# Optimization experiments

Measured on AMD Instinct MI355X. Metric: run time of the kernel, lower is better.

The kernel has to match this reference:

```python
import jax, jax.numpy as jnp
import numpy as np

# 2x2 string of 4 cores at these (h, w) positions; ring bond topology.
POS = [(0, 0), (0, 1), (1, 0), (1, 1)]
MIN_H, MAX_H = 0, 1
MIN_W, MAX_W = 0, 1
STD = 0.9  # DumbNormalInitialization std


def setup_inputs() -> dict:
    key = jax.random.key(0)
    k1, k2 = jax.random.split(key)
    # channels: first dim = in_num_channels (2), each [B, H, W, in_quantum]
    channels = jax.random.normal(k1, (2, 8, 128, 128, 4), dtype=jnp.float32)
    # cores: [n_cores, out_quantum, bond_left, bond_right, in_q0, in_q1]
    cores = STD * jax.random.normal(k2, (4, 2, 8, 8, 4, 4), dtype=jnp.float32)
    return {"channels": channels, "cores": cores}


def reference(channels, cores):
    ch0, ch1 = channels[0], channels[1]  # each [B, H, W, Qin]
    inters = []
    for i in range(4):
        # First stage: contract core's in_quantum dims with both channels per pixel
        # -> [B, out_q, H, W, bond_l, bond_r]
        t = jnp.einsum('qlrij,bhwi,bhwj->bqhwlr', cores[i], ch0, ch1)
        h, w = POS[i]
        pad_top = MAX_H - MIN_H - (h - MIN_H)
        pad_bot = h - MIN_H
        pad_left = MAX_W - MIN_W - (w - MIN_W)
        pad_right = w - MIN_W
        # pad spatial dims with value 1.0 (multiplicative identity)
        t = jnp.pad(
            t,
            ((0, 0), (0, 0), (pad_top, pad_bot), (pad_left, pad_right), (0, 0), (0, 0)),
            constant_values=1.0,
        )
        inters.append(t)
    # Second stage: ring contraction over bond dims (i->j->k->l->i)
    out = jnp.einsum('bphwij,bqhwjk,brhwkl,bshwli->bhwpqrs', *inters)
    B, Hp, Wp = out.shape[:3]
    out = out.reshape(B, Hp, Wp, -1)  # merge out_quantum dims
    dh = MAX_H - MIN_H
    dw = MAX_W - MIN_W
    return out[:, dh:Hp - dh, dw:Wp - dw, :]
```

## Files before the change

### kernel.cpp

```cpp
#include <hip/hip_runtime.h>


typedef __fp16 h2 __attribute__((ext_vector_type(2)));
typedef __fp16 h4 __attribute__((ext_vector_type(4)));
typedef float  f4 __attribute__((ext_vector_type(4)));

#define NB 8
#define NH 128
#define NW 128
#define HO 127
#define WO 127
#define CH1_OFF (NB*NH*NW*4)
#define PXSTR 664
#define ZOFF  648
#define CDROW 68
#define CDSTR 552
#define SS    20

#define PIN() asm volatile("" ::: "memory")
#define PKRTZ(a, b) __builtin_amdgcn_cvt_pkrtz((a), (b))

__device__ __forceinline__ f4 mfma16(h4 a, h4 b, f4 c) {
  return __builtin_amdgcn_mfma_f32_16x16x16f16(a, b, c, 0, 0, 0);
}

__global__ __launch_bounds__(256, 2)
void convsbs_fused(const float* __restrict__ ch,
                   const float* __restrict__ cores,
                   float* __restrict__ out) {
  const int tid  = threadIdx.x;
  const int lane = tid & 63;
  const int wid  = tid >> 6;
  const int quad = lane >> 4;
  const int nn   = lane & 15;
  const int x8   = lane & 7;
  const f4 F4Z = {0.f, 0.f, 0.f, 0.f};

  __shared__ __align__(16) __fp16 tlds[4][8 * PXSTR];
  __shared__ __align__(16) __fp16 cdlds[4][4 * CDSTR];
  __shared__ __align__(16) float  slds[4][4 * SS];
  __fp16* tbuf = tlds[wid];
  __fp16* cdb  = cdlds[wid];
  float*  sbuf = slds[wid];

  if (lane < 8) *(h4*)(tbuf + lane * PXSTR + ZOFF) = (h4){0, 0, 0, 0};
  PIN();

  __fp16* wrbase = tbuf + nn * PXSTR + quad * 4;
  const bool wr = (nn < 8);

  h4 wf[4][8];
#pragma unroll
  for (int c = 0; c < 4; ++c)
#pragma unroll
    for (int bi = 0; bi < 8; ++bi) {
      const int rowIdx = bi * 16 + nn;
      const int q  = rowIdx >> 6;
      const int ua = (rowIdx >> 3) & 7;
      const int ub = rowIdx & 7;
      const int l = (c & 1) ? ub : ua;
      const int r = (c & 1) ? ua : ub;
      const float4 wv = *(const float4*)(
          cores + ((((c * 2 + q) * 8 + l) * 8 + r) << 4) + quad * 4);
      h2 p0 = PKRTZ(wv.x, wv.y), p1 = PKRTZ(wv.z, wv.w);
      wf[c][bi] = (h4){p0[0], p0[1], p1[0], p1[1]};
    }

  const int hq = nn >> 3, hb = nn & 7;
  const int ctA = (quad < 2) ? ((2 + hq) * 80 + hb * 8 + quad * 4) : ZOFF;
  const int ctB = (quad < 2) ? ( hq      * 80 + hb * 8 + quad * 4) : ZOFF;
  const int dA  = (quad < 2) ? ((4 + hq) * 80 + hb * 8 + quad * 4) : ZOFF;
  const int dB  = (quad < 2) ? ((6 + hq) * 80 + hb * 8 + quad * 4) : ZOFF;
  const int ctW = (hq * 2 + (quad >> 1)) * CDROW + hb * 8 + (quad & 1) * 4;
  const int dW  = (4 + (quad >> 1) * 2 + hq) * CDROW + hb * 8 + (quad & 1) * 4;
  const int eA  = (nn >> 2) * CDSTR + (nn & 3) * CDROW + quad * 4;
  const int eB  = (nn >> 2) * CDSTR + (4 + (nn & 3)) * CDROW + quad * 4;
  const bool sW = ((nn >> 2) == quad);
  const int sWo = quad * SS + (nn & 3) * 4;
  const int sRo = quad * SS + (nn & 3) * 4 + (nn >> 2);

  const int blk = blockIdx.x;
  const int b = blk / 127;
  const int y = blk - b * 127;
  const int xq = wid * 32;
  const float* rowbase = ch + (size_t)((b * NH + y) * NW) * 4;
  float* obase = out + (size_t)((b * HO + y) * WO) * 16;

  float  a0[2][4];
  float4 a1[2][4];
  auto loadch = [&](int xtile, int bufi) {
#pragma unroll
    for (int c = 0; c < 4; ++c) {
      int col = xtile + x8 + (c & 1);
      col = col > 127 ? 127 : col;
      const float* cp = rowbase + (((c >> 1) * NW) + col) * 4;
      a0[bufi][c] = cp[quad];
      a1[bufi][c] = *(const float4*)(cp + CH1_OFF);
    }
  };

  loadch(xq, 0);

#pragma unroll
  for (int t = 0; t < 4; ++t) {
    const int cb = t & 1;

    h4 bf[4];
#pragma unroll
    for (int c = 0; c < 4; ++c) {
      const float s = a0[cb][c];
      const float4 v = a1[cb][c];
      h2 p0 = PKRTZ(s * v.x, s * v.y), p1 = PKRTZ(s * v.z, s * v.w);
      bf[c] = (h4){p0[0], p0[1], p1[0], p1[1]};
    }
    if (t < 3) loadch(xq + (t + 1) * 8, cb ^ 1);

#pragma unroll
    for (int c = 0; c < 4; ++c)
#pragma unroll
      for (int bi = 0; bi < 8; ++bi) {
        f4 acc = mfma16(wf[c][bi], bf[c], F4Z);
        h2 p0 = PKRTZ(acc[0], acc[1]), p1 = PKRTZ(acc[2], acc[3]);
        if (wr)
          *(h4*)(wrbase + c * 160 + bi * 16 + (bi >= 4 ? 16 : 0)) =
              (h4){p0[0], p0[1], p1[0], p1[1]};
      }
    PIN();

#pragma unroll
    for (int g = 0; g < 2; ++g) {
#pragma unroll
      for (int p4 = 0; p4 < 4; ++p4) {
        const __fp16* slot = tbuf + (g * 4 + p4) * PXSTR;
        __fp16* cd = cdb + p4 * CDSTR;
        h4 a1f = *(const h4*)(slot + ctA);
        h4 b1f = *(const h4*)(slot + ctB);
        f4 c0 = mfma16(a1f, b1f, F4Z);
        h2 u0 = PKRTZ(c0[0], c0[1]), u1 = PKRTZ(c0[2], c0[3]);
        *(h4*)(cd + ctW) = (h4){u0[0], u0[1], u1[0], u1[1]};
        h4 a2f = *(const h4*)(slot + dA);
        h4 b2f = *(const h4*)(slot + dB);
        f4 d0 = mfma16(a2f, b2f, F4Z);
        h2 v0 = PKRTZ(d0[0], d0[1]), v1 = PKRTZ(d0[2], d0[3]);
        *(h4*)(cd + dW) = (h4){v0[0], v0[1], v1[0], v1[1]};
      }
      PIN();

      f4 e = F4Z;
#pragma unroll
      for (int kb = 0; kb < 4; ++kb) {
        h4 ea = *(const h4*)(cdb + eA + kb * 16);
        h4 eb = *(const h4*)(cdb + eB + kb * 16);
        e = mfma16(ea, eb, e);
      }
      if (sW) *(float4*)(sbuf + sWo) = make_float4(e[0], e[1], e[2], e[3]);
      PIN();

      const float v = sbuf[sRo];
      const int x4 = xq + t * 8 + g * 4 + quad;
      if (x4 < WO) obase[x4 * 16 + nn] = v;
      PIN();
    }
  }
}

extern "C" void kernel_launch(void* const* d_in, const int* in_sizes, int n_in,
                              void* d_out, int out_size, void* d_ws, size_t ws_size,
                              hipStream_t stream) {
  (void)in_sizes; (void)n_in; (void)d_ws; (void)ws_size; (void)out_size;
  const float* ch    = (const float*)d_in[0];
  const float* cores = (const float*)d_in[1];
  float* out = (float*)d_out;
  convsbs_fused<<<8 * 127, 256, 0, stream>>>(ch, cores, out);
}
```

Baseline: 87.43 us.

## Split blocks into single-wave blocks, shrink LDS strides, split MFMA accumulator chain

The kernel now launches one 64-thread wave per block (four times as many blocks) instead of four waves sharing a 256-thread block, and changes launch bounds so more resident waves and finer scheduling are possible. LDS strides are reduced to cut the per-wave shared memory footprint. The final four-step dependent MFMA accumulation is split into two independent chains summed at the end, to shorten the dependency latency. Each block still loads the full core weights into registers, so the weight-conversion work per wave is unchanged, while block launch overhead grows and the new padding may change bank-conflict behaviour.

Result: slower. 95.65 us (+9.4%).

```diff
diff --git a/kernel.cpp b/kernel.cpp
--- a/kernel.cpp
+++ b/kernel.cpp
@@ -11,10 +11,10 @@
 #define HO 127
 #define WO 127
 #define CH1_OFF (NB*NH*NW*4)
-#define PXSTR 664
-#define ZOFF  648
+#define PXSTR 648
+#define ZOFF  640
 #define CDROW 68
-#define CDSTR 552
+#define CDSTR 544
 #define SS    20
 
 #define PIN() asm volatile("" ::: "memory")
@@ -24,24 +24,19 @@
   return __builtin_amdgcn_mfma_f32_16x16x16f16(a, b, c, 0, 0, 0);
 }
 
-__global__ __launch_bounds__(256, 2)
+__global__ __launch_bounds__(64, 3)
 void convsbs_fused(const float* __restrict__ ch,
                    const float* __restrict__ cores,
                    float* __restrict__ out) {
-  const int tid  = threadIdx.x;
-  const int lane = tid & 63;
-  const int wid  = tid >> 6;
+  const int lane = threadIdx.x & 63;
   const int quad = lane >> 4;
   const int nn   = lane & 15;
   const int x8   = lane & 7;
   const f4 F4Z = {0.f, 0.f, 0.f, 0.f};
 
-  __shared__ __align__(16) __fp16 tlds[4][8 * PXSTR];
-  __shared__ __align__(16) __fp16 cdlds[4][4 * CDSTR];
-  __shared__ __align__(16) float  slds[4][4 * SS];
-  __fp16* tbuf = tlds[wid];
-  __fp16* cdb  = cdlds[wid];
-  float*  sbuf = slds[wid];
+  __shared__ __align__(16) __fp16 tbuf[8 * PXSTR];
+  __shared__ __align__(16) __fp16 cdb[4 * CDSTR];
+  __shared__ __align__(16) float  sbuf[4 * SS];
 
   if (lane < 8) *(h4*)(tbuf + lane * PXSTR + ZOFF) = (h4){0, 0, 0, 0};
   PIN();
@@ -80,9 +75,10 @@
   const int sRo = quad * SS + (nn & 3) * 4 + (nn >> 2);
 
   const int blk = blockIdx.x;
-  const int b = blk / 127;
-  const int y = blk - b * 127;
-  const int xq = wid * 32;
+  const int by  = blk >> 2;
+  const int b   = by / 127;
+  const int y   = by - b * 127;
+  const int xq  = (blk & 3) * 32;
   const float* rowbase = ch + (size_t)((b * NH + y) * NW) * 4;
   float* obase = out + (size_t)((b * HO + y) * WO) * 16;
 
@@ -146,13 +142,20 @@
       }
       PIN();
 
-      f4 e = F4Z;
-#pragma unroll
-      for (int kb = 0; kb < 4; ++kb) {
-        h4 ea = *(const h4*)(cdb + eA + kb * 16);
-        h4 eb = *(const h4*)(cdb + eB + kb * 16);
-        e = mfma16(ea, eb, e);
+      f4 e0 = F4Z, e1 = F4Z;
+      {
+        h4 ea0 = *(const h4*)(cdb + eA);
+        h4 eb0 = *(const h4*)(cdb + eB);
+        h4 ea1 = *(const h4*)(cdb + eA + 16);
+        h4 eb1 = *(const h4*)(cdb + eB + 16);
+        h4 ea2 = *(const h4*)(cdb + eA + 32);
+        h4 eb2 = *(const h4*)(cdb + eB + 32);
+        h4 ea3 = *(const h4*)(cdb + eA + 48);
+        h4 eb3 = *(const h4*)(cdb + eB + 48);
+        e0 = mfma16(ea0, eb0, e0); e0 = mfma16(ea2, eb2, e0);
+        e1 = mfma16(ea1, eb1, e1); e1 = mfma16(ea3, eb3, e1);
       }
+      const f4 e = e0 + e1;
       if (sW) *(float4*)(sbuf + sWo) = make_float4(e[0], e[1], e[2], e[3]);
       PIN();
 
@@ -171,5 +174,5 @@
   const float* ch    = (const float*)d_in[0];
   const float* cores = (const float*)d_in[1];
   float* out = (float*)d_out;
-  convsbs_fused<<<8 * 127, 256, 0, stream>>>(ch, cores, out);
+  convsbs_fused<<<8 * 127 * 4, 64, 0, stream>>>(ch, cores, out);
 }
```
